# Kernel optimization log

Measured on AMD Instinct MI355X. Metric: run time of the kernel, lower is better.

## Reference

```python
import jax, jax.numpy as jnp
import numpy as np

NINP, NHID, NOUT = 400, 600, 400
HS = NHID + NOUT          # h_size = nhid + nout
NLEVELS, K, AUX_FREQ = 40, 2, 20
DILATION = [1]


def setup_inputs() -> dict:
    key = jax.random.key(0)
    ks = jax.random.split(key, 6)
    B, T = 8, 256
    bound = 0.01  # matches init_weights normal_(0, 0.01)
    return {
        "X": jax.random.normal(ks[0], (B, NINP, T), jnp.float32),
        "hid": jax.random.normal(ks[1], (B, HS, 1), jnp.float32),
        "cell": jax.random.normal(ks[2], (B, HS, 1), jnp.float32),
        "w1": jax.random.normal(ks[3], (4 * HS, NINP, K), jnp.float32) * bound,
        "w2": jax.random.normal(ks[4], (4 * HS, HS, K), jnp.float32) * bound,
        "b2": jax.random.normal(ks[5], (4 * HS,), jnp.float32) * bound,
    }


def _conv1d(x, w, d):
    # x: [B, Cin, T_padded], w: [Cout, Cin, K] -> [B, Cout, T]
    return jax.lax.conv_general_dilated(
        x, w, window_strides=(1,), padding='VALID', rhs_dilation=(d,),
        dimension_numbers=('NCH', 'OIH', 'NCH'))


def _forward(X, hid, cell, w1, w2, b2):
    B, _, T = X.shape
    ht = jnp.zeros((B, HS, T), X.dtype)
    ct = jnp.zeros((B, HS, T), X.dtype)

    # Input-side convolution is weight-tied and X never changes across levels,
    # so (like the torch dict cache) compute it once per distinct dilation.
    conv1 = {}
    for d in set(DILATION):
        pad = (K - 1) * d
        xp = jnp.pad(X, ((0, 0), (0, 0), (pad, 0)))
        conv1[d] = _conv1d(xp, w1, d)

    aux = []
    for i in range(NLEVELS):
        d = DILATION[i % len(DILATION)]
        pad = (K - 1) * d
        # causal left-pad of the hidden stream, filled with the initial hid
        z1 = jnp.concatenate([jnp.broadcast_to(hid, (B, HS, pad)), ht], axis=2)
        out = conv1[d] + _conv1d(z1, w2, d) + b2[None, :, None]  # [B, 4*HS, T]
        # shifted cell state, first d steps filled with the initial cell
        ct_1 = jnp.concatenate(
            [jnp.broadcast_to(cell, (B, HS, d)), ct[:, :, :-d]], axis=2)
        it = jax.nn.sigmoid(out[:, :HS])
        ot = jax.nn.sigmoid(out[:, HS:2 * HS])
        gt = jnp.tanh(out[:, 2 * HS:3 * HS])
        ft = jax.nn.sigmoid(out[:, 3 * HS:])
        ct = ft * ct_1 + it * gt
        ht = ot * jnp.tanh(ct)
        if i % AUX_FREQ == AUX_FREQ - 1:
            aux.append(ht[:, -NOUT:])  # [B, nout, T]

    out_main = jnp.transpose(ht[:, -NOUT:], (0, 2, 1))            # [B, T, nout]
    hc = (ht[:, :, -1:], ct[:, :, -1:])                            # ([B,HS,1], [B,HS,1])
    aux_outs = jnp.transpose(jnp.stack(aux, axis=0), (1, 0, 3, 2))  # [B, n_aux, T, nout]
    return out_main, hc, aux_outs


def reference(X, hid, cell, w1, w2, b2):
    return _forward(X, hid, cell, w1, w2, b2)
```

## Files before the change

### kernel.cpp

```cpp
#include <hip/hip_runtime.h>
#include <hip/hip_bf16.h>
#include <math.h>

typedef __bf16 bf16;
typedef __bf16 bf16x8 __attribute__((ext_vector_type(8)));
typedef __bf16 bf16x4 __attribute__((ext_vector_type(4)));
typedef float f32x4 __attribute__((ext_vector_type(4)));
typedef unsigned int u32;
typedef u32 u32x4 __attribute__((ext_vector_type(4)));

#define NINP 400
#define HS   1000
#define HP   1024
#define B_   8
#define T_   256
#define NT   2048
#define K2   2048
#define K1   1024
#define M_   4096

#define HT_OFF   819200
#define CT_OFF   827200
#define AUX_OFF  835200

typedef __attribute__((address_space(1))) const void gvoid;
typedef __attribute__((address_space(3))) void lvoid;

__device__ __forceinline__ void async_copy16(void* lds, const void* g) {
  __builtin_amdgcn_global_load_lds((gvoid*)g, (lvoid*)lds, 16, 0, 0);
}

__device__ __forceinline__ float sigm(float x) { return 1.0f / (1.0f + expf(-x)); }


__global__ void repack_w1(const float* __restrict__ w1, bf16* __restrict__ W1q) {
  int idx = blockIdx.x * 256 + threadIdx.x;
  if (idx >= M_ * K1) return;
  int pm = idx >> 10, k = idx & 1023;
  int g = (pm >> 4) & 3;
  int h = (pm >> 7) * 32 + ((pm >> 6) & 1) * 16 + (pm & 15);
  float v = 0.0f;
  if (h < HS) {
    int c = g * HS + h;
    if (k < 512) { if (k < NINP) v = w1[(size_t)c * (NINP * 2) + k * 2 + 0]; }
    else { int j = k - 512; if (j < NINP) v = w1[(size_t)c * (NINP * 2) + j * 2 + 1]; }
  }
  W1q[idx] = (bf16)v;
}

__global__ void repack_w2(const float* __restrict__ w2, bf16* __restrict__ W2q) {
  int idx = blockIdx.x * 256 + threadIdx.x;
  if (idx >= M_ * K2) return;
  int pm = idx >> 11, k = idx & 2047;
  int g = (pm >> 4) & 3;
  int h = (pm >> 7) * 32 + ((pm >> 6) & 1) * 16 + (pm & 15);
  float v = 0.0f;
  if (h < HS) {
    int c = g * HS + h;
    if (k < HP) { if (k < HS) v = w2[(size_t)c * (HS * 2) + k * 2 + 0]; }
    else { int j = k - HP; if (j < HS) v = w2[(size_t)c * (HS * 2) + j * 2 + 1]; }
  }
  W2q[idx] = (bf16)v;
}

__global__ void build_xt(const float* __restrict__ X, bf16* __restrict__ XT) {
  int idx = blockIdx.x * 256 + threadIdx.x;
  if (idx >= NT * K1) return;
  int n = idx >> 10, k = idx & 1023;
  int b = n >> 8, t = n & (T_ - 1);
  float v = 0.0f;
  if (k < 512) { if (k < NINP && t > 0) v = X[((size_t)b * NINP + k) * T_ + t - 1]; }
  else { int j = k - 512; if (j < NINP) v = X[((size_t)b * NINP + j) * T_ + t]; }
  XT[idx] = (bf16)v;
}

__global__ void build_hc(const float* __restrict__ hid, const float* __restrict__ cell,
                         bf16* __restrict__ hidp, float* __restrict__ cellp) {
  int idx = blockIdx.x * 256 + threadIdx.x;
  if (idx >= B_ * HP) return;
  int b = idx >> 10, k = idx & (HP - 1);
  hidp[idx]  = (k < HS) ? (bf16)hid[b * HS + k] : (bf16)0.0f;
  cellp[idx] = (k < HS) ? cell[b * HS + k] : 0.0f;
}


template <bool GATED>
__global__ __launch_bounds__(256, 2) void gemm_step(
    const bf16* __restrict__ A,
    const bf16* __restrict__ Bsrc,
    const bf16* __restrict__ hidp,
    const bf16* __restrict__ CbIn,
    bf16* __restrict__ CbOut,
    const float* __restrict__ b2,
    const bf16* __restrict__ ctprev,
    const float* __restrict__ cellp,
    bf16* __restrict__ ctnew,
    bf16* __restrict__ Hnew,
    int K) {
  __shared__ bf16 As[2][128][64];
  __shared__ bf16 Bs[2][128][64];

  const int tid = threadIdx.x;
  const int lane = tid & 63;
  const int w = tid >> 6;
  const int mh = w >> 1, nh = w & 1;
  const int dr = lane >> 3, c8 = lane & 7;
  const int swo = ((c8 - dr) & 7) * 8;
  const int quad = lane >> 4, col = lane & 15;

  const int L = blockIdx.y * gridDim.x + blockIdx.x;
  const int bm = (L & 7) * 4 + (L >> 7);
  const int n0 = ((L >> 3) & 15) * 128;

  bf16x4 cb0[4], cb1[4], cb2[4], cb3[4];
  if (GATED) {
#pragma unroll
    for (int nt = 0; nt < 4; ++nt) {
      const int n = n0 + nh * 64 + nt * 16 + col;
      const size_t cb = (size_t)n * 4096 + (size_t)(bm * 128 + mh * 64) + quad * 4;
      cb0[nt] = *(const bf16x4*)&CbIn[cb + 0];
      cb1[nt] = *(const bf16x4*)&CbIn[cb + 16];
      cb2[nt] = *(const bf16x4*)&CbIn[cb + 32];
      cb3[nt] = *(const bf16x4*)&CbIn[cb + 48];
    }
  }

  const bf16* pa[4];
  const bf16* pb_lo[4];
  const bf16* pb_hi[4];
#pragma unroll
  for (int j = 0; j < 4; ++j) {
    const int r = j * 32 + w * 8 + dr;
    pa[j] = A + (size_t)(bm * 128 + r) * K + swo;
    const int n = n0 + r;
    if (GATED) {
      const int t = n & (T_ - 1);
      pb_lo[j] = (t == 0) ? (hidp + (size_t)(n >> 8) * HP + swo)
                          : (Bsrc + (size_t)(n - 1) * HP + swo);
      pb_hi[j] = Bsrc + (size_t)n * HP + swo - HP;
    } else {
      pb_lo[j] = Bsrc + (size_t)n * K + swo;
      pb_hi[j] = pb_lo[j];
    }
  }

  f32x4 acc[4][4];
#pragma unroll
  for (int i = 0; i < 4; ++i)
#pragma unroll
    for (int j = 0; j < 4; ++j) acc[i][j] = (f32x4){0.f, 0.f, 0.f, 0.f};

  auto stage = [&](int buf, int it2) {
#pragma unroll
    for (int j = 0; j < 4; ++j)
      async_copy16(&As[buf][j * 32 + w * 8][0], pa[j] + it2 * 64);
#pragma unroll
    for (int j = 0; j < 4; ++j) {
      const bf16* src = (GATED && it2 >= 16) ? pb_hi[j] : pb_lo[j];
      async_copy16(&Bs[buf][j * 32 + w * 8][0], src + it2 * 64);
    }
  };

  const int NIT = K >> 6;

  auto kstep = [&](int it2, int buf) {
    {
      bf16x8 av[4], bv[4];
#pragma unroll
      for (int mt = 0; mt < 4; ++mt) {
        const int rA = mh * 64 + mt * 16 + col;
        av[mt] = *(const bf16x8*)&As[buf][rA][((quad + rA) & 7) * 8];
      }
#pragma unroll
      for (int nt = 0; nt < 4; ++nt) {
        const int rB = nh * 64 + nt * 16 + col;
        bv[nt] = *(const bf16x8*)&Bs[buf][rB][((quad + rB) & 7) * 8];
      }
      __builtin_amdgcn_s_barrier();
      asm volatile("s_waitcnt lgkmcnt(0)" ::: "memory");
      __builtin_amdgcn_sched_barrier(0);
      __builtin_amdgcn_s_setprio(1);
#pragma unroll
      for (int mt = 0; mt < 4; ++mt)
#pragma unroll
        for (int nt = 0; nt < 4; ++nt)
          acc[mt][nt] = __builtin_amdgcn_mfma_f32_16x16x32_bf16(av[mt], bv[nt], acc[mt][nt], 0, 0, 0);
      __builtin_amdgcn_s_setprio(0);
      __builtin_amdgcn_s_barrier();
    }
    {
      bf16x8 av[4], bv[4];
#pragma unroll
      for (int mt = 0; mt < 4; ++mt) {
        const int rA = mh * 64 + mt * 16 + col;
        av[mt] = *(const bf16x8*)&As[buf][rA][((4 + quad + rA) & 7) * 8];
      }
#pragma unroll
      for (int nt = 0; nt < 4; ++nt) {
        const int rB = nh * 64 + nt * 16 + col;
        bv[nt] = *(const bf16x8*)&Bs[buf][rB][((4 + quad + rB) & 7) * 8];
      }
      asm volatile("s_waitcnt lgkmcnt(0)" ::: "memory");
      __builtin_amdgcn_sched_barrier(0);
      __builtin_amdgcn_s_barrier();
      if (it2 + 2 < NIT) {
        stage(buf, it2 + 2);
        asm volatile("s_waitcnt vmcnt(8)" ::: "memory");
      } else {
        asm volatile("s_waitcnt vmcnt(0)" ::: "memory");
      }
      __builtin_amdgcn_sched_barrier(0);
      __builtin_amdgcn_s_setprio(1);
#pragma unroll
      for (int mt = 0; mt < 4; ++mt)
#pragma unroll
        for (int nt = 0; nt < 4; ++nt)
          acc[mt][nt] = __builtin_amdgcn_mfma_f32_16x16x32_bf16(av[mt], bv[nt], acc[mt][nt], 0, 0, 0);
      __builtin_amdgcn_s_setprio(0);
      __builtin_amdgcn_s_barrier();
    }
  };

  stage(0, 0);
  stage(1, 1);
  asm volatile("s_waitcnt vmcnt(8)" ::: "memory");
  __builtin_amdgcn_s_barrier();

  for (int it2 = 0; it2 < NIT; it2 += 2) {
    kstep(it2, 0);
    kstep(it2 + 1, 1);
  }
  __syncthreads();

  if (!GATED) {
    bf16 (*Csh)[128] = (bf16(*)[128])&As[0][0][0];
#pragma unroll
    for (int mt = 0; mt < 4; ++mt) {
#pragma unroll
      for (int nt = 0; nt < 4; ++nt) {
        const int nloc = nh * 64 + nt * 16 + col;
        bf16x4 v;
#pragma unroll
        for (int j = 0; j < 4; ++j) {
          const int h = bm * 32 + mh * 16 + quad * 4 + j;
          const float bias = (h < HS) ? b2[mt * HS + h] : 0.0f;
          v[j] = (bf16)(acc[mt][nt][j] + bias);
        }
        *(bf16x4*)&Csh[nloc][mh * 64 + mt * 16 + quad * 4] = v;
      }
    }
    __syncthreads();
#pragma unroll
    for (int i2 = 0; i2 < 8; ++i2) {
      const int idx = i2 * 256 + tid;
      const int rrow = idx >> 4, off = idx & 15;
      *(u32x4*)&CbOut[(size_t)(n0 + rrow) * 4096 + bm * 128 + off * 8] =
          *(const u32x4*)&Csh[rrow][off * 8];
    }
  } else {
    bf16 (*Hsh)[32] = (bf16(*)[32])&As[0][0][0];
#pragma unroll
    for (int nt = 0; nt < 4; ++nt) {
      const int nloc = nh * 64 + nt * 16 + col;
      const int n = n0 + nloc;
      const int b = n >> 8;
      const int t = n & (T_ - 1);
      bf16x4 hv;
#pragma unroll
      for (int j = 0; j < 4; ++j) {
        const int h = bm * 32 + mh * 16 + quad * 4 + j;
        const float ci = acc[0][nt][j] + (float)cb0[nt][j];
        const float co = acc[1][nt][j] + (float)cb1[nt][j];
        const float cg = acc[2][nt][j] + (float)cb2[nt][j];
        const float cf = acc[3][nt][j] + (float)cb3[nt][j];
        const float ctold = (t == 0) ? cellp[b * HP + h]
                                     : (float)ctprev[(size_t)h * NT + (n - 1)];
        const float cn = sigm(cf) * ctold + sigm(ci) * tanhf(cg);
        ctnew[(size_t)h * NT + n] = (bf16)cn;
        hv[j] = (bf16)(sigm(co) * tanhf(cn));
      }
      *(bf16x4*)&Hsh[nloc][mh * 16 + quad * 4] = hv;
    }
    __syncthreads();
#pragma unroll
    for (int i2 = 0; i2 < 2; ++i2) {
      const int idx = i2 * 256 + tid;
      const int rrow = idx >> 2, off = idx & 3;
      *(u32x4*)&Hnew[(size_t)(n0 + rrow) * HP + bm * 32 + off * 8] =
          *(const u32x4*)&Hsh[rrow][off * 8];
    }
  }
}


__global__ void aux_kernel(const bf16* __restrict__ H, float* __restrict__ out, int s) {
  int idx = blockIdx.x * 256 + threadIdx.x;
  if (idx >= NT * 100) return;
  int n = idx / 100;
  int o = (idx % 100) * 4;
  int b = n >> 8, t = n & (T_ - 1);
  bf16x4 v = *(const bf16x4*)&H[(size_t)n * HP + 600 + o];
  f32x4 f = {(float)v[0], (float)v[1], (float)v[2], (float)v[3]};
  *(f32x4*)&out[AUX_OFF + ((size_t)((b * 2 + s) * T_ + t)) * 400 + o] = f;
}

__global__ void final_kernel(const bf16* __restrict__ H, const bf16* __restrict__ ct,
                             float* __restrict__ out) {
  int idx = blockIdx.x * 256 + threadIdx.x;
  if (idx < NT * 100) {
    int n = idx / 100;
    int o = (idx % 100) * 4;
    int b = n >> 8, t = n & (T_ - 1);
    bf16x4 v = *(const bf16x4*)&H[(size_t)n * HP + 600 + o];
    f32x4 f = {(float)v[0], (float)v[1], (float)v[2], (float)v[3]};
    *(f32x4*)&out[(size_t)n * 400 + o] = f;
    *(f32x4*)&out[AUX_OFF + ((size_t)((b * 2 + 1) * T_ + t)) * 400 + o] = f;
  } else {
    int j = idx - NT * 100;
    if (j < 8000) {
      int b = j / 1000, h = j % 1000;
      out[HT_OFF + j] = (float)H[(size_t)(b * T_ + 255) * HP + h];
    } else if (j < 16000) {
      int jj = j - 8000;
      int b = jj / 1000, h = jj % 1000;
      out[CT_OFF + jj] = (float)ct[(size_t)h * NT + b * T_ + 255];
    }
  }
}


extern "C" void kernel_launch(void* const* d_in, const int* in_sizes, int n_in,
                              void* d_out, int out_size, void* d_ws, size_t ws_size,
                              hipStream_t stream) {
  const float* X    = (const float*)d_in[0];
  const float* hid  = (const float*)d_in[1];
  const float* cell = (const float*)d_in[2];
  const float* w1   = (const float*)d_in[3];
  const float* w2   = (const float*)d_in[4];
  const float* b2   = (const float*)d_in[5];
  float* out = (float*)d_out;

  char* ws = (char*)d_ws;
  size_t off = 0;
  auto alloc = [&](size_t bytes) {
    void* p = ws + off;
    off += (bytes + 255) & ~(size_t)255;
    return p;
  };
  bf16* W2q    = (bf16*)alloc((size_t)M_ * K2 * 2);
  bf16* CbP    = (bf16*)alloc((size_t)NT * M_ * 2);
  bf16* Hb0    = (bf16*)alloc((size_t)NT * HP * 2);
  bf16* ctb0   = (bf16*)alloc((size_t)HP * NT * 2);
  bf16* hidp   = (bf16*)alloc((size_t)B_ * HP * 2);
  float* cellp = (float*)alloc((size_t)B_ * HP * 4);
  char* R = (char*)alloc((size_t)12 * 1024 * 1024);
  bf16* W1q  = (bf16*)R;
  bf16* XT   = (bf16*)(R + (size_t)8 * 1024 * 1024);
  bf16* ctb1 = (bf16*)R;
  bf16* Hb1  = (bf16*)(R + (size_t)4 * 1024 * 1024);

  bf16* Hb[2]  = {Hb0, Hb1};
  bf16* ctb[2] = {ctb0, ctb1};

  hipMemsetAsync(Hb[0], 0, (size_t)NT * HP * 2, stream);
  hipMemsetAsync(ctb[0], 0, (size_t)HP * NT * 2, stream);

  repack_w1<<<(M_ * K1) / 256, 256, 0, stream>>>(w1, W1q);
  repack_w2<<<(M_ * K2) / 256, 256, 0, stream>>>(w2, W2q);
  build_xt<<<(NT * K1) / 256, 256, 0, stream>>>(X, XT);
  build_hc<<<(B_ * HP) / 256, 256, 0, stream>>>(hid, cell, hidp, cellp);

  dim3 grid(NT / 128, M_ / 128);
  gemm_step<false><<<grid, 256, 0, stream>>>(W1q, XT, nullptr, nullptr, CbP, b2,
                                             nullptr, nullptr, nullptr, nullptr, K1);
  for (int i = 0; i < 40; ++i) {
    int p = i & 1;
    gemm_step<true><<<grid, 256, 0, stream>>>(W2q, Hb[p], hidp, CbP, nullptr, nullptr,
                                              ctb[p], cellp, ctb[p ^ 1], Hb[p ^ 1], K2);
    if (i == 19) aux_kernel<<<800, 256, 0, stream>>>(Hb[p ^ 1], out, 0);
  }
  final_kernel<<<(NT * 100 + 16000 + 255) / 256, 256, 0, stream>>>(Hb[0], ctb[0], out);
}
```

Before: 1.965 ms.

## Share one B tile across both conv taps via row-shifted LDS reads

```diff
diff --git a/kernel.cpp b/kernel.cpp
--- a/kernel.cpp
+++ b/kernel.cpp
@@ -15,8 +15,6 @@
 #define B_   8
 #define T_   256
 #define NT   2048
-#define K2   2048
-#define K1   1024
 #define M_   4096
 
 #define HT_OFF   819200
@@ -35,7 +33,7 @@
 
 __global__ void repack_w1(const float* __restrict__ w1, bf16* __restrict__ W1q) {
   int idx = blockIdx.x * 256 + threadIdx.x;
-  if (idx >= M_ * K1) return;
+  if (idx >= M_ * 1024) return;
   int pm = idx >> 10, k = idx & 1023;
   int g = (pm >> 4) & 3;
   int h = (pm >> 7) * 32 + ((pm >> 6) & 1) * 16 + (pm & 15);
@@ -50,7 +48,7 @@
 
 __global__ void repack_w2(const float* __restrict__ w2, bf16* __restrict__ W2q) {
   int idx = blockIdx.x * 256 + threadIdx.x;
-  if (idx >= M_ * K2) return;
+  if (idx >= M_ * 2048) return;
   int pm = idx >> 11, k = idx & 2047;
   int g = (pm >> 4) & 3;
   int h = (pm >> 7) * 32 + ((pm >> 6) & 1) * 16 + (pm & 15);
@@ -63,15 +61,14 @@
   W2q[idx] = (bf16)v;
 }
 
-__global__ void build_xt(const float* __restrict__ X, bf16* __restrict__ XT) {
-  int idx = blockIdx.x * 256 + threadIdx.x;
-  if (idx >= NT * K1) return;
-  int n = idx >> 10, k = idx & 1023;
+__global__ void build_xs(const float* __restrict__ X, bf16* __restrict__ XS) {
+  int idx = blockIdx.x * 256 + threadIdx.x;
+  if (idx >= NT * 512) return;
+  int n = idx >> 9, k = idx & 511;
   int b = n >> 8, t = n & (T_ - 1);
   float v = 0.0f;
-  if (k < 512) { if (k < NINP && t > 0) v = X[((size_t)b * NINP + k) * T_ + t - 1]; }
-  else { int j = k - 512; if (j < NINP) v = X[((size_t)b * NINP + j) * T_ + t]; }
-  XT[idx] = (bf16)v;
+  if (k < NINP) v = X[((size_t)b * NINP + k) * T_ + t];
+  XS[idx] = (bf16)v;
 }
 
 __global__ void build_hc(const float* __restrict__ hid, const float* __restrict__ cell,
@@ -96,17 +93,16 @@
     const float* __restrict__ cellp,
     bf16* __restrict__ ctnew,
     bf16* __restrict__ Hnew,
-    int K) {
-  __shared__ bf16 As[2][128][64];
-  __shared__ bf16 Bs[2][128][64];
+    int KH, int BS) {
+  __shared__ bf16 SM[2][3][4096];
+  __shared__ __align__(16) bf16 H0row[1024];
 
   const int tid = threadIdx.x;
   const int lane = tid & 63;
   const int w = tid >> 6;
   const int mh = w >> 1, nh = w & 1;
-  const int dr = lane >> 3, c8 = lane & 7;
-  const int swo = ((c8 - dr) & 7) * 8;
   const int quad = lane >> 4, col = lane & 15;
+  const int K = KH * 2;
 
   const int L = blockIdx.y * gridDim.x + blockIdx.x;
   const int bm = (L & 7) * 4 + (L >> 7);
@@ -125,23 +121,29 @@
     }
   }
 
-  const bf16* pa[4];
-  const bf16* pb_lo[4];
-  const bf16* pb_hi[4];
-#pragma unroll
-  for (int j = 0; j < 4; ++j) {
-    const int r = j * 32 + w * 8 + dr;
-    pa[j] = A + (size_t)(bm * 128 + r) * K + swo;
-    const int n = n0 + r;
-    if (GATED) {
-      const int t = n & (T_ - 1);
-      pb_lo[j] = (t == 0) ? (hidp + (size_t)(n >> 8) * HP + swo)
-                          : (Bsrc + (size_t)(n - 1) * HP + swo);
-      pb_hi[j] = Bsrc + (size_t)n * HP + swo - HP;
-    } else {
-      pb_lo[j] = Bsrc + (size_t)n * K + swo;
-      pb_hi[j] = pb_lo[j];
-    }
+  const int colh = col >> 1;
+  const int slotA = ((quad + 4 * (col & 1) + (colh & 7)) & 7) * 8;
+  const int baseA   = (mh * 32 + colh) * 64 + slotA;
+  const int baseBhi = (nh * 32 + colh) * 64 + slotA;
+  const bool useH0 = (nh == 0 && col == 0);
+  int baseLo[4];
+#pragma unroll
+  for (int nt = 0; nt < 4; ++nt) {
+    const int r = nh * 64 + nt * 16 + col - 1;
+    const int pr = r >> 1;
+    baseLo[nt] = pr * 64 + (((quad + 4 * (r & 1) + (pr & 7)) & 7) * 8);
+  }
+
+  const bf16* paLo[2];
+  const bf16* pbs[2];
+#pragma unroll
+  for (int l = 0; l < 2; ++l) {
+    const int f = l * 256 + tid;
+    const int pr = f >> 3, sl = f & 7;
+    const int u = (sl - (pr & 7)) & 7;
+    const int r = 2 * pr + (u >> 2), k8 = u & 3;
+    paLo[l] = A + (size_t)(bm * 128 + r) * K + k8 * 8;
+    pbs[l]  = Bsrc + (size_t)(n0 + r) * BS + k8 * 8;
   }
 
   f32x4 acc[4][4];
@@ -150,32 +152,31 @@
 #pragma unroll
     for (int j = 0; j < 4; ++j) acc[i][j] = (f32x4){0.f, 0.f, 0.f, 0.f};
 
-  auto stage = [&](int buf, int it2) {
-#pragma unroll
-    for (int j = 0; j < 4; ++j)
-      async_copy16(&As[buf][j * 32 + w * 8][0], pa[j] + it2 * 64);
-#pragma unroll
-    for (int j = 0; j < 4; ++j) {
-      const bf16* src = (GATED && it2 >= 16) ? pb_hi[j] : pb_lo[j];
-      async_copy16(&Bs[buf][j * 32 + w * 8][0], src + it2 * 64);
+  auto stage = [&](int buf, int p2) {
+#pragma unroll
+    for (int l = 0; l < 2; ++l) {
+      async_copy16(&SM[buf][0][(l * 256 + w * 64) * 8], paLo[l] + p2 * 32);
+      async_copy16(&SM[buf][1][(l * 256 + w * 64) * 8], paLo[l] + KH + p2 * 32);
+      async_copy16(&SM[buf][2][(l * 256 + w * 64) * 8], pbs[l] + p2 * 32);
     }
   };
 
-  const int NIT = K >> 6;
-
-  auto kstep = [&](int it2, int buf) {
+  const int NP = KH >> 5;
+
+  auto kpair = [&](int p2, int buf) {
     {
       bf16x8 av[4], bv[4];
 #pragma unroll
-      for (int mt = 0; mt < 4; ++mt) {
-        const int rA = mh * 64 + mt * 16 + col;
-        av[mt] = *(const bf16x8*)&As[buf][rA][((quad + rA) & 7) * 8];
+      for (int mt = 0; mt < 4; ++mt)
+        av[mt] = *(const bf16x8*)&SM[buf][0][baseA + mt * 512];
+      {
+        const bf16* p0 = useH0 ? &H0row[p2 * 32 + quad * 8]
+                               : &SM[buf][2][baseLo[0]];
+        bv[0] = *(const bf16x8*)p0;
       }
 #pragma unroll
-      for (int nt = 0; nt < 4; ++nt) {
-        const int rB = nh * 64 + nt * 16 + col;
-        bv[nt] = *(const bf16x8*)&Bs[buf][rB][((quad + rB) & 7) * 8];
-      }
+      for (int nt = 1; nt < 4; ++nt)
+        bv[nt] = *(const bf16x8*)&SM[buf][2][baseLo[nt]];
       __builtin_amdgcn_s_barrier();
       asm volatile("s_waitcnt lgkmcnt(0)" ::: "memory");
       __builtin_amdgcn_sched_barrier(0);
@@ -191,21 +192,17 @@
     {
       bf16x8 av[4], bv[4];
 #pragma unroll
-      for (int mt = 0; mt < 4; ++mt) {
-        const int rA = mh * 64 + mt * 16 + col;
-        av[mt] = *(const bf16x8*)&As[buf][rA][((4 + quad + rA) & 7) * 8];
-      }
-#pragma unroll
-      for (int nt = 0; nt < 4; ++nt) {
-        const int rB = nh * 64 + nt * 16 + col;
-        bv[nt] = *(const bf16x8*)&Bs[buf][rB][((4 + quad + rB) & 7) * 8];
-      }
+      for (int mt = 0; mt < 4; ++mt)
+        av[mt] = *(const bf16x8*)&SM[buf][1][baseA + mt * 512];
+#pragma unroll
+      for (int nt = 0; nt < 4; ++nt)
+        bv[nt] = *(const bf16x8*)&SM[buf][2][baseBhi + nt * 512];
       asm volatile("s_waitcnt lgkmcnt(0)" ::: "memory");
       __builtin_amdgcn_sched_barrier(0);
       __builtin_amdgcn_s_barrier();
-      if (it2 + 2 < NIT) {
-        stage(buf, it2 + 2);
-        asm volatile("s_waitcnt vmcnt(8)" ::: "memory");
+      if (p2 + 2 < NP) {
+        stage(buf, p2 + 2);
+        asm volatile("s_waitcnt vmcnt(6)" ::: "memory");
       } else {
         asm volatile("s_waitcnt vmcnt(0)" ::: "memory");
       }
@@ -221,19 +218,32 @@
     }
   };
 
+  if (GATED) {
+    if (w < 2) {
+      const bf16* s = ((n0 & 255) == 0)
+          ? (hidp + (size_t)(n0 >> 8) * HP + lane * 8 + w * 512)
+          : (Bsrc + (size_t)(n0 - 1) * BS + lane * 8 + w * 512);
+      async_copy16(&H0row[w * 512], s);
+    }
+  } else {
+    if ((n0 & 255) == 0) {
+      if (tid < 64) *(u32x4*)&H0row[tid * 8] = (u32x4){0, 0, 0, 0};
+    } else if (w < 1) {
+      async_copy16(&H0row[w * 512], Bsrc + (size_t)(n0 - 1) * BS + lane * 8 + w * 512);
+    }
+  }
   stage(0, 0);
   stage(1, 1);
-  asm volatile("s_waitcnt vmcnt(8)" ::: "memory");
-  __builtin_amdgcn_s_barrier();
-
-  for (int it2 = 0; it2 < NIT; it2 += 2) {
-    kstep(it2, 0);
-    kstep(it2 + 1, 1);
-  }
   __syncthreads();
 
+  for (int p = 0; p < NP; p += 2) {
+    kpair(p, 0);
+    kpair(p + 1, 1);
+  }
+  __syncthreads();
+
   if (!GATED) {
-    bf16 (*Csh)[128] = (bf16(*)[128])&As[0][0][0];
+    bf16 (*Csh)[128] = (bf16(*)[128])&SM[0][0][0];
 #pragma unroll
     for (int mt = 0; mt < 4; ++mt) {
 #pragma unroll
@@ -258,7 +268,7 @@
           *(const u32x4*)&Csh[rrow][off * 8];
     }
   } else {
-    bf16 (*Hsh)[32] = (bf16(*)[32])&As[0][0][0];
+    bf16 (*Hsh)[32] = (bf16(*)[32])&SM[0][0][0];
 #pragma unroll
     for (int nt = 0; nt < 4; ++nt) {
       const int nloc = nh * 64 + nt * 16 + col;
@@ -347,7 +357,7 @@
     off += (bytes + 255) & ~(size_t)255;
     return p;
   };
-  bf16* W2q    = (bf16*)alloc((size_t)M_ * K2 * 2);
+  bf16* W2q    = (bf16*)alloc((size_t)M_ * 2048 * 2);
   bf16* CbP    = (bf16*)alloc((size_t)NT * M_ * 2);
   bf16* Hb0    = (bf16*)alloc((size_t)NT * HP * 2);
   bf16* ctb0   = (bf16*)alloc((size_t)HP * NT * 2);
@@ -355,7 +365,7 @@
   float* cellp = (float*)alloc((size_t)B_ * HP * 4);
   char* R = (char*)alloc((size_t)12 * 1024 * 1024);
   bf16* W1q  = (bf16*)R;
-  bf16* XT   = (bf16*)(R + (size_t)8 * 1024 * 1024);
+  bf16* XS   = (bf16*)(R + (size_t)8 * 1024 * 1024);
   bf16* ctb1 = (bf16*)R;
   bf16* Hb1  = (bf16*)(R + (size_t)4 * 1024 * 1024);
 
@@ -365,18 +375,20 @@
   hipMemsetAsync(Hb[0], 0, (size_t)NT * HP * 2, stream);
   hipMemsetAsync(ctb[0], 0, (size_t)HP * NT * 2, stream);
 
-  repack_w1<<<(M_ * K1) / 256, 256, 0, stream>>>(w1, W1q);
-  repack_w2<<<(M_ * K2) / 256, 256, 0, stream>>>(w2, W2q);
-  build_xt<<<(NT * K1) / 256, 256, 0, stream>>>(X, XT);
+  repack_w1<<<(M_ * 1024) / 256, 256, 0, stream>>>(w1, W1q);
+  repack_w2<<<(M_ * 2048) / 256, 256, 0, stream>>>(w2, W2q);
+  build_xs<<<(NT * 512) / 256, 256, 0, stream>>>(X, XS);
   build_hc<<<(B_ * HP) / 256, 256, 0, stream>>>(hid, cell, hidp, cellp);
 
   dim3 grid(NT / 128, M_ / 128);
-  gemm_step<false><<<grid, 256, 0, stream>>>(W1q, XT, nullptr, nullptr, CbP, b2,
-                                             nullptr, nullptr, nullptr, nullptr, K1);
+  gemm_step<false><<<grid, 256, 0, stream>>>(W1q, XS, nullptr, nullptr, CbP, b2,
+                                             nullptr, nullptr, nullptr, nullptr,
+                                             512, 512);
   for (int i = 0; i < 40; ++i) {
     int p = i & 1;
     gemm_step<true><<<grid, 256, 0, stream>>>(W2q, Hb[p], hidp, CbP, nullptr, nullptr,
-                                              ctb[p], cellp, ctb[p ^ 1], Hb[p ^ 1], K2);
+                                              ctb[p], cellp, ctb[p ^ 1], Hb[p ^ 1],
+                                              1024, 1024);
     if (i == 19) aux_kernel<<<800, 256, 0, stream>>>(Hb[p ^ 1], out, 0);
   }
   final_kernel<<<(NT * 100 + 16000 + 255) / 256, 256, 0, stream>>>(Hb[0], ctb[0], out);
```

Result: no change. 1.957 ms (-0.4%).
